# Kernel optimization log

Hardware: AMD Instinct MI355X
Metric: run time of the kernel (lower is better)

The kernel has to match this reference:

```python
import jax, jax.numpy as jnp
import numpy as np

N = 100000
E = 1600000
D_IN = 128
D_H = 128


def setup_inputs() -> dict:
    key = jax.random.key(0)
    ks = jax.random.split(key, 8)
    x = jax.random.normal(ks[0], (N, D_IN), dtype=jnp.float32)
    edge_index = jax.random.randint(ks[1], (2, E), 0, N, dtype=jnp.int64)
    edge_weights = jax.random.uniform(ks[2], (E,), dtype=jnp.float32)
    # GCNConv params (glorot-ish scale), bias zeros like PyG default init reset
    W1 = jax.random.normal(ks[3], (D_IN, D_H), dtype=jnp.float32) / np.sqrt(D_IN)
    b1 = jnp.zeros((D_H,), dtype=jnp.float32)
    W2 = jax.random.normal(ks[4], (D_H, D_H), dtype=jnp.float32) / np.sqrt(D_H)
    b2 = jnp.zeros((D_H,), dtype=jnp.float32)
    a_prelu = jnp.full((D_H,), 0.25, dtype=jnp.float32)  # nn.PReLU(hidden_dim)
    return {"x": x, "edge_index": edge_index, "edge_weights": edge_weights,
            "W1": W1, "b1": b1, "W2": W2, "b2": b2, "a_prelu": a_prelu}


def _gcn_norm(edge_index, edge_weights, n_nodes):
    # add self loops (weight 1), symmetric normalization deg^-1/2 A deg^-1/2
    loop = jnp.arange(n_nodes, dtype=edge_index.dtype)
    src = jnp.concatenate([edge_index[0], loop])
    dst = jnp.concatenate([edge_index[1], loop])
    w = jnp.concatenate([edge_weights, jnp.ones((n_nodes,), edge_weights.dtype)])
    deg = jax.ops.segment_sum(w, dst, num_segments=n_nodes)
    dis = jnp.where(deg > 0, jax.lax.rsqrt(jnp.maximum(deg, 1e-12)), 0.0)
    norm = dis[src] * w * dis[dst]
    return src, dst, norm


def _gcn_layer(h, W, b, src, dst, norm, n_nodes):
    h = h @ W                                   # [N, D] linear (no bias)
    msg = h[src] * norm[:, None]                # gather + scale  [E+N, D]
    out = jax.ops.segment_sum(msg, dst, num_segments=n_nodes)
    return out + b


def _prelu(z, a):
    return jnp.where(z >= 0, z, a * z)


def reference(x, edge_index, edge_weights, W1, b1, W2, b2, a_prelu):
    n = x.shape[0]
    src, dst, norm = _gcn_norm(edge_index, edge_weights, n)
    z = _prelu(_gcn_layer(x, W1, b1, src, dst, norm, n), a_prelu)
    z = _prelu(_gcn_layer(z, W2, b2, src, dst, norm, n), a_prelu)
    return z
```

## Files before the change

kernel.cpp:

```cpp
#include <hip/hip_runtime.h>
#include <hip/hip_fp16.h>

#define D 128
#define CAP 64
#define NBKT 512
#define CHUNK 4096
#define BKTCAP 5120

typedef _Float16 f16x8 __attribute__((ext_vector_type(8)));
typedef float f32x4 __attribute__((ext_vector_type(4)));

__global__ __launch_bounds__(256) void k_conv(const float2* __restrict__ X,
        const float* __restrict__ dis, __half2* __restrict__ Xh, int m) {
    int i = blockIdx.x * 256 + threadIdx.x;
    if (i < m) {
        float dv = dis[i >> 6];
        float2 f = X[i];
        Xh[i] = __floats2half2_rn(dv * f.x, dv * f.y);
    }
}

__global__ __launch_bounds__(256) void k_bin(const int* __restrict__ ei,
        const float* __restrict__ ew, int* __restrict__ gcur,
        int2* __restrict__ gbkt, int e) {
    __shared__ int hist[NBKT];
    __shared__ int base[NBKT];
    int t = threadIdx.x;
    int b0 = blockIdx.x * CHUNK;
    int cnt = min(CHUNK, e - b0);
    for (int i = t; i < NBKT; i += 256) hist[i] = 0;
    __syncthreads();
    int meta[16]; float w[16]; int pos[16]; int bkt[16];
    #pragma unroll
    for (int j = 0; j < 16; ++j) {
        int li = t + j * 256;
        bkt[j] = -1;
        if (li < cnt) {
            int i = b0 + li;
            int d = ei[e + i];
            int s = ei[i];
            bkt[j] = d >> 8;
            meta[j] = s | ((d & 255) << 24);
            w[j] = ew[i];
            pos[j] = atomicAdd(&hist[bkt[j]], 1);
        }
    }
    __syncthreads();
    for (int i = t; i < NBKT; i += 256)
        if (hist[i] > 0) base[i] = atomicAdd(&gcur[i], hist[i]);
    __syncthreads();
    #pragma unroll
    for (int j = 0; j < 16; ++j) {
        if (bkt[j] >= 0) {
            int idx = base[bkt[j]] + pos[j];
            if (idx < BKTCAP)
                gbkt[(size_t)bkt[j] * BKTCAP + idx] =
                    make_int2(meta[j], __float_as_int(w[j]));
        }
    }
}

__global__ __launch_bounds__(256) void k_scat2(const int2* __restrict__ gbkt,
        const int* __restrict__ gcur, int* cursor, int2* __restrict__ slot,
        float* __restrict__ dis, int n) {
    int bkt = blockIdx.x;
    int nodebase = bkt << 8;
    if (nodebase >= n) return;
    int cnt = min(gcur[bkt], BKTCAP);
    int t = threadIdx.x;
    for (int i = t; i < cnt; i += 256) {
        int2 r = gbkt[(size_t)bkt * BKTCAP + i];
        int d = nodebase | ((unsigned)r.x >> 24);
        int s = r.x & 0xFFFFFF;
        int pos = atomicAdd(&cursor[d], 1);
        if (pos < CAP) slot[(size_t)d * CAP + pos] = make_int2(s, r.y);
    }
    __syncthreads();
    int v = nodebase + t;
    if (v < n) {
        int c = min(atomicAdd(&cursor[v], 0), CAP);
        const int2* row = slot + (size_t)v * CAP;
        float wsum = 0.f;
        for (int i = 0; i < c; ++i) wsum += __int_as_float(row[i].y);
        dis[v] = rsqrtf(1.0f + wsum);
    }
}

__global__ __launch_bounds__(256) void k_agg(const __half2* __restrict__ Hs,
        const int2* __restrict__ slot, const int* __restrict__ cursor,
        const float* __restrict__ dis, __half2* __restrict__ out, int n) {
    int wid = threadIdx.x >> 6, lane = threadIdx.x & 63;
    int v = blockIdx.x * 4 + wid;
    if (v >= n) return;
    int half = lane >> 5;
    int m = lane & 31;
    int c = min(cursor[v], CAP);
    int c1 = c + 1;
    const int2* row = slot + (size_t)v * CAP;
    const __half* Hb = (const __half*)Hs;

    float4 acc = make_float4(0.f, 0.f, 0.f, 0.f);
    for (int i = 0; i < c1; i += 8) {
        int2 e[4];
        #pragma unroll
        for (int k = 0; k < 4; ++k) {
            int j = i + 2 * k + half;
            int jj = j - 1;
            jj = (jj < 0) ? 0 : (jj >= CAP ? CAP - 1 : jj);
            int2 ld = row[jj];
            bool real = (j >= 1) && (j < c1);
            int2 ee;
            ee.x = real ? (ld.x & 0xFFFFFF) : v;
            ee.y = real ? ld.y : ((j == 0) ? 0x3f800000 : 0);
            e[k] = ee;
        }
        float2 g[4];
        #pragma unroll
        for (int k = 0; k < 4; ++k)
            g[k] = *(const float2*)(Hb + ((size_t)e[k].x << 7) + (m << 2));
        #pragma unroll
        for (int k = 0; k < 4; ++k) {
            float w = __int_as_float(e[k].y);
            union { float2 f; __half2 h[2]; } u; u.f = g[k];
            float2 lo = __half22float2(u.h[0]);
            float2 hi = __half22float2(u.h[1]);
            acc.x = fmaf(w, lo.x, acc.x);
            acc.y = fmaf(w, lo.y, acc.y);
            acc.z = fmaf(w, hi.x, acc.z);
            acc.w = fmaf(w, hi.y, acc.w);
        }
    }
    acc.x += __shfl_xor(acc.x, 32);
    acc.y += __shfl_xor(acc.y, 32);
    acc.z += __shfl_xor(acc.z, 32);
    acc.w += __shfl_xor(acc.w, 32);
    if (half == 0) {
        float dv = dis[v];
        union { float2 f; __half2 h[2]; } o;
        o.h[0] = __floats2half2_rn(dv * acc.x, dv * acc.y);
        o.h[1] = __floats2half2_rn(dv * acc.z, dv * acc.w);
        *(float2*)((__half*)out + ((size_t)v << 7) + (m << 2)) = o.f;
    }
}

__global__ __launch_bounds__(256) void k_packW(const float* __restrict__ W,
        __half* __restrict__ Wpk) {
    int idx = blockIdx.x * 256 + threadIdx.x;
    if (idx >= 2048) return;
    int lane = idx & 63, nt = (idx >> 6) & 7, ks = idx >> 9;
    int col = nt * 16 + (lane & 15);
    int kb = ks * 32 + (lane >> 4) * 8;
    #pragma unroll
    for (int j = 0; j < 8; ++j)
        Wpk[idx * 8 + j] = __float2half(W[(kb + j) * D + col]);
}

template <bool HALF_OUT>
__global__ __launch_bounds__(256) void k_gemm(const __half* __restrict__ A,
        const __half* __restrict__ Wpk, const float* __restrict__ b,
        const float* __restrict__ ap, const float* __restrict__ dis,
        void* __restrict__ Cv, int n) {
    int t = threadIdx.x;
    int wv = t >> 6, lane = t & 63;
    int base = blockIdx.x * 64 + wv * 16;
    int row = base + (lane & 15);
    int rowc = min(row, n - 1);
    int kg = lane >> 4;

    const f16x8* Arow = (const f16x8*)(A + (size_t)rowc * D);
    f16x8 afr[4];
    #pragma unroll
    for (int ks = 0; ks < 4; ++ks) afr[ks] = Arow[ks * 4 + kg];

    const f16x8* Wp = (const f16x8*)Wpk;
    f32x4 acc[8];
    #pragma unroll
    for (int nt = 0; nt < 8; ++nt) acc[nt] = (f32x4){0.f, 0.f, 0.f, 0.f};

    #pragma unroll
    for (int ks = 0; ks < 4; ++ks) {
        #pragma unroll
        for (int nt = 0; nt < 8; ++nt) {
            f16x8 bfr = Wp[(ks * 8 + nt) * 64 + lane];
            acc[nt] = __builtin_amdgcn_mfma_f32_16x16x32_f16(afr[ks], bfr, acc[nt], 0, 0, 0);
        }
    }

    int c0 = lane & 15;
    int r0 = base + (lane >> 4) * 4;
    float dv[4];
    #pragma unroll
    for (int q = 0; q < 4; ++q)
        dv[q] = HALF_OUT ? dis[min(r0 + q, n - 1)] : 1.0f;
    #pragma unroll
    for (int nt = 0; nt < 8; ++nt) {
        int col = nt * 16 + c0;
        float bb = b[col], aa = ap[col];
        #pragma unroll
        for (int q = 0; q < 4; ++q) {
            int r = r0 + q;
            if (r < n) {
                float z = acc[nt][q] + bb;
                z = (z >= 0.f) ? z : aa * z;
                if (HALF_OUT) ((__half*)Cv)[(size_t)r * D + col] = __float2half(dv[q] * z);
                else          ((float*)Cv)[(size_t)r * D + col] = z;
            }
        }
    }
}


extern "C" void kernel_launch(void* const* d_in, const int* in_sizes, int n_in,
                              void* d_out, int out_size, void* d_ws, size_t ws_size,
                              hipStream_t stream) {
    const float* x  = (const float*)d_in[0];
    const int*   ei = (const int*)d_in[1];
    const float* ew = (const float*)d_in[2];
    const float* W1 = (const float*)d_in[3];
    const float* b1 = (const float*)d_in[4];
    const float* W2 = (const float*)d_in[5];
    const float* b2 = (const float*)d_in[6];
    const float* ap = (const float*)d_in[7];

    int n = in_sizes[0] / D;
    int e = in_sizes[2];

    int*     cursor = (int*)d_ws;
    int*     gcur   = cursor + n;
    float*   dis    = (float*)(gcur + NBKT);
    int2*    gbkt   = (int2*)(dis + n);
    int2*    slot   = gbkt + (size_t)NBKT * BKTCAP;
    __half2* xh     = (__half2*)(slot + (size_t)n * CAP);
    __half2* ah     = xh + (size_t)n * 64;
    __half*  Wpk1   = (__half*)(ah + (size_t)n * 64);
    __half*  Wpk2   = Wpk1 + 16384;
    float*   out    = (float*)d_out;

    int nbw = (n + 3) / 4;
    int nbg = (n + 63) / 64;
    int nbin = (e + CHUNK - 1) / CHUNK;

    hipMemsetAsync(cursor, 0, (size_t)(n + NBKT) * sizeof(int), stream);
    k_bin<<<nbin, 256, 0, stream>>>(ei, ew, gcur, gbkt, e);
    k_scat2<<<NBKT, 256, 0, stream>>>(gbkt, gcur, cursor, slot, dis, n);
    k_conv<<<(n * 64 + 255) / 256, 256, 0, stream>>>((const float2*)x, dis, xh, n * 64);
    k_packW<<<8, 256, 0, stream>>>(W1, Wpk1);
    k_packW<<<8, 256, 0, stream>>>(W2, Wpk2);

    k_agg<<<nbw, 256, 0, stream>>>(xh, slot, cursor, dis, ah, n);
    k_gemm<true><<<nbg, 256, 0, stream>>>((const __half*)ah, Wpk1, b1, ap, dis, (void*)xh, n);
    k_agg<<<nbw, 256, 0, stream>>>(xh, slot, cursor, dis, ah, n);
    k_gemm<false><<<nbg, 256, 0, stream>>>((const __half*)ah, Wpk2, b2, ap, dis, (void*)out, n);
}
```

Baseline: 265.8 us.

## Fuse neighbor aggregation into GEMM via LDS and compact packed CSR metadata

Aggregation and the MFMA GEMM now run in one kernel: each wave aggregates 16 rows into an LDS tile and feeds that tile straight to the MFMA, so the intermediate aggregated matrix no longer makes a round trip through global memory. The scatter kernel also builds a compact CSR-style array of 4-byte entries (17-bit source plus fp16 weight) using a block prefix scan, replacing the 8-byte padded slots. Edge metadata is loaded once per row and broadcast with shuffles. The cost is lower per-row parallelism in the gather loop, a 17-bit node-index limit, weights rounded to fp16, and the degree cap lowered to 62.

```diff
diff --git a/kernel.cpp b/kernel.cpp
--- a/kernel.cpp
+++ b/kernel.cpp
@@ -62,7 +62,9 @@
 
 __global__ __launch_bounds__(256) void k_scat2(const int2* __restrict__ gbkt,
         const int* __restrict__ gcur, int* cursor, int2* __restrict__ slot,
+        unsigned* __restrict__ meta, int* __restrict__ rsc,
         float* __restrict__ dis, int n) {
+    __shared__ int sscan[256];
     int bkt = blockIdx.x;
     int nodebase = bkt << 8;
     if (nodebase >= n) return;
@@ -77,69 +79,33 @@
     }
     __syncthreads();
     int v = nodebase + t;
+    int c = 0;
     if (v < n) {
-        int c = min(atomicAdd(&cursor[v], 0), CAP);
+        c = min(atomicAdd(&cursor[v], 0), 62);
         const int2* row = slot + (size_t)v * CAP;
         float wsum = 0.f;
         for (int i = 0; i < c; ++i) wsum += __int_as_float(row[i].y);
         dis[v] = rsqrtf(1.0f + wsum);
     }
-}
-
-__global__ __launch_bounds__(256) void k_agg(const __half2* __restrict__ Hs,
-        const int2* __restrict__ slot, const int* __restrict__ cursor,
-        const float* __restrict__ dis, __half2* __restrict__ out, int n) {
-    int wid = threadIdx.x >> 6, lane = threadIdx.x & 63;
-    int v = blockIdx.x * 4 + wid;
-    if (v >= n) return;
-    int half = lane >> 5;
-    int m = lane & 31;
-    int c = min(cursor[v], CAP);
-    int c1 = c + 1;
-    const int2* row = slot + (size_t)v * CAP;
-    const __half* Hb = (const __half*)Hs;
-
-    float4 acc = make_float4(0.f, 0.f, 0.f, 0.f);
-    for (int i = 0; i < c1; i += 8) {
-        int2 e[4];
-        #pragma unroll
-        for (int k = 0; k < 4; ++k) {
-            int j = i + 2 * k + half;
-            int jj = j - 1;
-            jj = (jj < 0) ? 0 : (jj >= CAP ? CAP - 1 : jj);
-            int2 ld = row[jj];
-            bool real = (j >= 1) && (j < c1);
-            int2 ee;
-            ee.x = real ? (ld.x & 0xFFFFFF) : v;
-            ee.y = real ? ld.y : ((j == 0) ? 0x3f800000 : 0);
-            e[k] = ee;
-        }
-        float2 g[4];
-        #pragma unroll
-        for (int k = 0; k < 4; ++k)
-            g[k] = *(const float2*)(Hb + ((size_t)e[k].x << 7) + (m << 2));
-        #pragma unroll
-        for (int k = 0; k < 4; ++k) {
-            float w = __int_as_float(e[k].y);
-            union { float2 f; __half2 h[2]; } u; u.f = g[k];
-            float2 lo = __half22float2(u.h[0]);
-            float2 hi = __half22float2(u.h[1]);
-            acc.x = fmaf(w, lo.x, acc.x);
-            acc.y = fmaf(w, lo.y, acc.y);
-            acc.z = fmaf(w, hi.x, acc.z);
-            acc.w = fmaf(w, hi.y, acc.w);
-        }
-    }
-    acc.x += __shfl_xor(acc.x, 32);
-    acc.y += __shfl_xor(acc.y, 32);
-    acc.z += __shfl_xor(acc.z, 32);
-    acc.w += __shfl_xor(acc.w, 32);
-    if (half == 0) {
-        float dv = dis[v];
-        union { float2 f; __half2 h[2]; } o;
-        o.h[0] = __floats2half2_rn(dv * acc.x, dv * acc.y);
-        o.h[1] = __floats2half2_rn(dv * acc.z, dv * acc.w);
-        *(float2*)((__half*)out + ((size_t)v << 7) + (m << 2)) = o.f;
+    sscan[t] = c;
+    __syncthreads();
+    int val = c;
+    for (int off = 1; off < 256; off <<= 1) {
+        int tmp = (t >= off) ? sscan[t - off] : 0;
+        __syncthreads();
+        sscan[t] += tmp;
+        __syncthreads();
+    }
+    if (v < n) {
+        int myoff = sscan[t] - val;
+        int mb = bkt * BKTCAP + myoff;
+        rsc[v] = mb | (c << 24);
+        const int2* row = slot + (size_t)v * CAP;
+        for (int i = 0; i < c; ++i) {
+            int2 sw = row[i];
+            unsigned hb = (unsigned)__half_as_ushort(__float2half(__int_as_float(sw.y)));
+            meta[mb + i] = (unsigned)sw.x | (hb << 17);
+        }
     }
 }
 
@@ -156,27 +122,74 @@
 }
 
 template <bool HALF_OUT>
-__global__ __launch_bounds__(256) void k_gemm(const __half* __restrict__ A,
-        const __half* __restrict__ Wpk, const float* __restrict__ b,
-        const float* __restrict__ ap, const float* __restrict__ dis,
+__global__ __launch_bounds__(256) void k_fused(const __half* __restrict__ Hs,
+        const unsigned* __restrict__ meta, const int* __restrict__ rsc,
+        const float* __restrict__ dis, const __half* __restrict__ Wpk,
+        const float* __restrict__ bias, const float* __restrict__ ap,
         void* __restrict__ Cv, int n) {
-    int t = threadIdx.x;
-    int wv = t >> 6, lane = t & 63;
+    __shared__ __half As[4][16][136];
+    int t = threadIdx.x, wv = t >> 6, lane = t & 63;
     int base = blockIdx.x * 64 + wv * 16;
-    int row = base + (lane & 15);
-    int rowc = min(row, n - 1);
+    int half = lane >> 5, m = lane & 31;
+    const char* Hb = (const char*)Hs;
+
+    for (int r = 0; r < 16; ++r) {
+        int v = base + r;
+        float4 a0 = make_float4(0.f, 0.f, 0.f, 0.f);
+        float4 a1 = make_float4(0.f, 0.f, 0.f, 0.f);
+        float dv = 0.f;
+        if (v < n) {
+            dv = dis[v];
+            int rc = rsc[v];
+            int rs = rc & 0xFFFFFF;
+            int c1 = (int)((unsigned)rc >> 24) + 1;
+            unsigned mm;
+            if (lane == 0) mm = (unsigned)v | (0x3C00u << 17);
+            else if (lane < c1) mm = meta[rs + lane - 1];
+            else mm = (unsigned)v;
+            int voff = (int)(mm & 0x1FFFFu) << 8;
+            float wf = __half2float(__ushort_as_half((unsigned short)(mm >> 17)));
+            for (int j0 = 0; j0 < c1; j0 += 4) {
+                int sl0 = j0 + half, sl1 = j0 + 2 + half;
+                int vo0 = __shfl(voff, sl0);
+                float w0 = __shfl(wf, sl0);
+                int vo1 = __shfl(voff, sl1);
+                float w1 = __shfl(wf, sl1);
+                float2 g0 = *(const float2*)(Hb + vo0 + (m << 3));
+                float2 g1 = *(const float2*)(Hb + vo1 + (m << 3));
+                union { float2 f; __half2 h[2]; } u0, u1;
+                u0.f = g0; u1.f = g1;
+                float2 l0 = __half22float2(u0.h[0]), h0 = __half22float2(u0.h[1]);
+                float2 l1 = __half22float2(u1.h[0]), h1 = __half22float2(u1.h[1]);
+                a0.x = fmaf(w0, l0.x, a0.x); a0.y = fmaf(w0, l0.y, a0.y);
+                a0.z = fmaf(w0, h0.x, a0.z); a0.w = fmaf(w0, h0.y, a0.w);
+                a1.x = fmaf(w1, l1.x, a1.x); a1.y = fmaf(w1, l1.y, a1.y);
+                a1.z = fmaf(w1, h1.x, a1.z); a1.w = fmaf(w1, h1.y, a1.w);
+            }
+        }
+        a0.x += a1.x; a0.y += a1.y; a0.z += a1.z; a0.w += a1.w;
+        a0.x += __shfl_xor(a0.x, 32);
+        a0.y += __shfl_xor(a0.y, 32);
+        a0.z += __shfl_xor(a0.z, 32);
+        a0.w += __shfl_xor(a0.w, 32);
+        if (half == 0) {
+            union { float2 f; __half2 h[2]; } o;
+            o.h[0] = __floats2half2_rn(dv * a0.x, dv * a0.y);
+            o.h[1] = __floats2half2_rn(dv * a0.z, dv * a0.w);
+            *(float2*)(&As[wv][r][m << 2]) = o.f;
+        }
+    }
+
     int kg = lane >> 4;
-
-    const f16x8* Arow = (const f16x8*)(A + (size_t)rowc * D);
     f16x8 afr[4];
     #pragma unroll
-    for (int ks = 0; ks < 4; ++ks) afr[ks] = Arow[ks * 4 + kg];
+    for (int ks = 0; ks < 4; ++ks)
+        afr[ks] = *(const f16x8*)(&As[wv][lane & 15][ks * 32 + kg * 8]);
 
     const f16x8* Wp = (const f16x8*)Wpk;
     f32x4 acc[8];
     #pragma unroll
     for (int nt = 0; nt < 8; ++nt) acc[nt] = (f32x4){0.f, 0.f, 0.f, 0.f};
-
     #pragma unroll
     for (int ks = 0; ks < 4; ++ks) {
         #pragma unroll
@@ -195,7 +208,7 @@
     #pragma unroll
     for (int nt = 0; nt < 8; ++nt) {
         int col = nt * 16 + c0;
-        float bb = b[col], aa = ap[col];
+        float bb = bias[col], aa = ap[col];
         #pragma unroll
         for (int q = 0; q < 4; ++q) {
             int r = r0 + q;
@@ -225,30 +238,31 @@
     int n = in_sizes[0] / D;
     int e = in_sizes[2];
 
-    int*     cursor = (int*)d_ws;
-    int*     gcur   = cursor + n;
-    float*   dis    = (float*)(gcur + NBKT);
-    int2*    gbkt   = (int2*)(dis + n);
-    int2*    slot   = gbkt + (size_t)NBKT * BKTCAP;
-    __half2* xh     = (__half2*)(slot + (size_t)n * CAP);
-    __half2* ah     = xh + (size_t)n * 64;
-    __half*  Wpk1   = (__half*)(ah + (size_t)n * 64);
-    __half*  Wpk2   = Wpk1 + 16384;
-    float*   out    = (float*)d_out;
-
-    int nbw = (n + 3) / 4;
+    int*      cursor = (int*)d_ws;
+    int*      gcur   = cursor + n;
+    float*    dis    = (float*)(gcur + NBKT);
+    int*      rsc    = (int*)(dis + n);
+    int2*     gbkt   = (int2*)(rsc + n);
+    int2*     slot   = gbkt + (size_t)NBKT * BKTCAP;
+    unsigned* meta   = (unsigned*)(slot + (size_t)n * CAP);
+    __half2*  xh     = (__half2*)(meta + (size_t)NBKT * BKTCAP);
+    __half2*  z1h    = xh + (size_t)n * 64;
+    __half*   Wpk1   = (__half*)(z1h + (size_t)n * 64);
+    __half*   Wpk2   = Wpk1 + 16384;
+    float*    out    = (float*)d_out;
+
+    int nbin = (e + CHUNK - 1) / CHUNK;
     int nbg = (n + 63) / 64;
-    int nbin = (e + CHUNK - 1) / CHUNK;
 
     hipMemsetAsync(cursor, 0, (size_t)(n + NBKT) * sizeof(int), stream);
     k_bin<<<nbin, 256, 0, stream>>>(ei, ew, gcur, gbkt, e);
-    k_scat2<<<NBKT, 256, 0, stream>>>(gbkt, gcur, cursor, slot, dis, n);
+    k_scat2<<<NBKT, 256, 0, stream>>>(gbkt, gcur, cursor, slot, meta, rsc, dis, n);
     k_conv<<<(n * 64 + 255) / 256, 256, 0, stream>>>((const float2*)x, dis, xh, n * 64);
     k_packW<<<8, 256, 0, stream>>>(W1, Wpk1);
     k_packW<<<8, 256, 0, stream>>>(W2, Wpk2);
 
-    k_agg<<<nbw, 256, 0, stream>>>(xh, slot, cursor, dis, ah, n);
-    k_gemm<true><<<nbg, 256, 0, stream>>>((const __half*)ah, Wpk1, b1, ap, dis, (void*)xh, n);
-    k_agg<<<nbw, 256, 0, stream>>>(xh, slot, cursor, dis, ah, n);
-    k_gemm<false><<<nbg, 256, 0, stream>>>((const __half*)ah, Wpk2, b2, ap, dis, (void*)out, n);
-}
+    k_fused<true><<<nbg, 256, 0, stream>>>((const __half*)xh, meta, rsc, dis,
+                                           Wpk1, b1, ap, (void*)z1h, n);
+    k_fused<false><<<nbg, 256, 0, stream>>>((const __half*)z1h, meta, rsc, dis,
+                                            Wpk2, b2, ap, (void*)out, n);
+}
```

Result: slower. 310.8 us (+16.9%).

## Replace fixed-capacity per-node slots with compact CSR built in-block, fuse conversion

Applied to the files above, without the earlier changes.

Rebuilds the per-bucket scatter so that each block histograms its 256 destination nodes in shared memory, prefix-scans the counts, and writes edges into a compact CSR-like array packed with a row offset and count per node. This replaces the fixed 64-slot per-node layout and its global atomics and per-node memset. Degree-weight sums are accumulated in shared memory, and the fp16 conversion of x is folded into the same kernel. The two weight-pack launches are merged into one, and layer-1 output now goes to a separate buffer. Counts are clamped at 255, and the gather in aggregation becomes more compact and cache friendly.

```diff
diff --git a/kernel.cpp b/kernel.cpp
--- a/kernel.cpp
+++ b/kernel.cpp
@@ -2,23 +2,12 @@
 #include <hip/hip_fp16.h>
 
 #define D 128
-#define CAP 64
 #define NBKT 512
 #define CHUNK 4096
 #define BKTCAP 5120
 
 typedef _Float16 f16x8 __attribute__((ext_vector_type(8)));
 typedef float f32x4 __attribute__((ext_vector_type(4)));
-
-__global__ __launch_bounds__(256) void k_conv(const float2* __restrict__ X,
-        const float* __restrict__ dis, __half2* __restrict__ Xh, int m) {
-    int i = blockIdx.x * 256 + threadIdx.x;
-    if (i < m) {
-        float dv = dis[i >> 6];
-        float2 f = X[i];
-        Xh[i] = __floats2half2_rn(dv * f.x, dv * f.y);
-    }
-}
 
 __global__ __launch_bounds__(256) void k_bin(const int* __restrict__ ei,
         const float* __restrict__ ew, int* __restrict__ gcur,
@@ -61,42 +50,76 @@
 }
 
 __global__ __launch_bounds__(256) void k_scat2(const int2* __restrict__ gbkt,
-        const int* __restrict__ gcur, int* cursor, int2* __restrict__ slot,
-        float* __restrict__ dis, int n) {
+        const int* __restrict__ gcur, const float2* __restrict__ X,
+        int2* __restrict__ meta, int* __restrict__ rsc, float* __restrict__ dis,
+        __half2* __restrict__ xh, int n) {
+    __shared__ int hist[256];
+    __shared__ int cur[256];
+    __shared__ int scn[256];
+    __shared__ int basearr[256];
+    __shared__ float wsum[256];
+    __shared__ float disv[256];
     int bkt = blockIdx.x;
     int nodebase = bkt << 8;
-    if (nodebase >= n) return;
+    int t = threadIdx.x;
     int cnt = min(gcur[bkt], BKTCAP);
-    int t = threadIdx.x;
+    hist[t] = 0; cur[t] = 0; wsum[t] = 0.f;
+    __syncthreads();
     for (int i = t; i < cnt; i += 256) {
         int2 r = gbkt[(size_t)bkt * BKTCAP + i];
-        int d = nodebase | ((unsigned)r.x >> 24);
-        int s = r.x & 0xFFFFFF;
-        int pos = atomicAdd(&cursor[d], 1);
-        if (pos < CAP) slot[(size_t)d * CAP + pos] = make_int2(s, r.y);
-    }
-    __syncthreads();
+        int dl = (unsigned)r.x >> 24;
+        atomicAdd(&hist[dl], 1);
+        atomicAdd(&wsum[dl], __int_as_float(r.y));
+    }
+    __syncthreads();
+    int c = hist[t];
+    scn[t] = c;
+    __syncthreads();
+    for (int off = 1; off < 256; off <<= 1) {
+        int tmp = (t >= off) ? scn[t - off] : 0;
+        __syncthreads();
+        scn[t] += tmp;
+        __syncthreads();
+    }
+    int myoff = scn[t] - c;
+    basearr[t] = myoff;
+    __syncthreads();
+    for (int i = t; i < cnt; i += 256) {
+        int2 r = gbkt[(size_t)bkt * BKTCAP + i];
+        int dl = (unsigned)r.x >> 24;
+        int pos = atomicAdd(&cur[dl], 1);
+        meta[(size_t)bkt * BKTCAP + basearr[dl] + pos] =
+            make_int2(r.x & 0xFFFFFF, r.y);
+    }
     int v = nodebase + t;
+    float dv = 1.f;
     if (v < n) {
-        int c = min(atomicAdd(&cursor[v], 0), CAP);
-        const int2* row = slot + (size_t)v * CAP;
-        float wsum = 0.f;
-        for (int i = 0; i < c; ++i) wsum += __int_as_float(row[i].y);
-        dis[v] = rsqrtf(1.0f + wsum);
+        dv = rsqrtf(1.0f + wsum[t]);
+        dis[v] = dv;
+        rsc[v] = (bkt * BKTCAP + myoff) | (min(c, 255) << 24);
+    }
+    disv[t] = dv;
+    __syncthreads();
+    int nrow = min(256, n - nodebase);
+    size_t rowbase = (size_t)nodebase << 6;
+    for (int idx = t; idx < nrow * 64; idx += 256) {
+        float dv2 = disv[idx >> 6];
+        float2 f = X[rowbase + idx];
+        xh[rowbase + idx] = __floats2half2_rn(dv2 * f.x, dv2 * f.y);
     }
 }
 
 __global__ __launch_bounds__(256) void k_agg(const __half2* __restrict__ Hs,
-        const int2* __restrict__ slot, const int* __restrict__ cursor,
+        const int2* __restrict__ meta, const int* __restrict__ rsc,
         const float* __restrict__ dis, __half2* __restrict__ out, int n) {
     int wid = threadIdx.x >> 6, lane = threadIdx.x & 63;
     int v = blockIdx.x * 4 + wid;
     if (v >= n) return;
     int half = lane >> 5;
     int m = lane & 31;
-    int c = min(cursor[v], CAP);
-    int c1 = c + 1;
-    const int2* row = slot + (size_t)v * CAP;
+    int rc = rsc[v];
+    int c1 = (int)((unsigned)rc >> 24) + 1;
+    const int2* row = meta + (rc & 0xFFFFFF);
     const __half* Hb = (const __half*)Hs;
 
     float4 acc = make_float4(0.f, 0.f, 0.f, 0.f);
@@ -106,11 +129,11 @@
         for (int k = 0; k < 4; ++k) {
             int j = i + 2 * k + half;
             int jj = j - 1;
-            jj = (jj < 0) ? 0 : (jj >= CAP ? CAP - 1 : jj);
+            jj = (jj < 0) ? 0 : jj;
             int2 ld = row[jj];
             bool real = (j >= 1) && (j < c1);
             int2 ee;
-            ee.x = real ? (ld.x & 0xFFFFFF) : v;
+            ee.x = real ? ld.x : v;
             ee.y = real ? ld.y : ((j == 0) ? 0x3f800000 : 0);
             e[k] = ee;
         }
@@ -143,16 +166,20 @@
     }
 }
 
-__global__ __launch_bounds__(256) void k_packW(const float* __restrict__ W,
-        __half* __restrict__ Wpk) {
-    int idx = blockIdx.x * 256 + threadIdx.x;
-    if (idx >= 2048) return;
+__global__ __launch_bounds__(256) void k_packW(const float* __restrict__ W1,
+        const float* __restrict__ W2, __half* __restrict__ Wpk1,
+        __half* __restrict__ Wpk2) {
+    int gidx = blockIdx.x * 256 + threadIdx.x;
+    if (gidx >= 4096) return;
+    const float* W = (gidx < 2048) ? W1 : W2;
+    __half* P = (gidx < 2048) ? Wpk1 : Wpk2;
+    int idx = gidx & 2047;
     int lane = idx & 63, nt = (idx >> 6) & 7, ks = idx >> 9;
     int col = nt * 16 + (lane & 15);
     int kb = ks * 32 + (lane >> 4) * 8;
     #pragma unroll
     for (int j = 0; j < 8; ++j)
-        Wpk[idx * 8 + j] = __float2half(W[(kb + j) * D + col]);
+        P[idx * 8 + j] = __float2half(W[(kb + j) * D + col]);
 }
 
 template <bool HALF_OUT>
@@ -225,30 +252,30 @@
     int n = in_sizes[0] / D;
     int e = in_sizes[2];
 
-    int*     cursor = (int*)d_ws;
-    int*     gcur   = cursor + n;
-    float*   dis    = (float*)(gcur + NBKT);
-    int2*    gbkt   = (int2*)(dis + n);
-    int2*    slot   = gbkt + (size_t)NBKT * BKTCAP;
-    __half2* xh     = (__half2*)(slot + (size_t)n * CAP);
-    __half2* ah     = xh + (size_t)n * 64;
-    __half*  Wpk1   = (__half*)(ah + (size_t)n * 64);
-    __half*  Wpk2   = Wpk1 + 16384;
-    float*   out    = (float*)d_out;
-
-    int nbw = (n + 3) / 4;
-    int nbg = (n + 63) / 64;
+    int*     gcur = (int*)d_ws;
+    float*   dis  = (float*)(gcur + NBKT);
+    int*     rsc  = (int*)(dis + n);
+    int2*    gbkt = (int2*)(rsc + n);
+    int2*    meta = gbkt + (size_t)NBKT * BKTCAP;
+    __half2* xh   = (__half2*)(meta + (size_t)NBKT * BKTCAP + 256);
+    __half2* z1h  = xh + (size_t)n * 64;
+    __half2* ah   = z1h + (size_t)n * 64;
+    __half*  Wpk1 = (__half*)(ah + (size_t)n * 64);
+    __half*  Wpk2 = Wpk1 + 16384;
+    float*   out  = (float*)d_out;
+
     int nbin = (e + CHUNK - 1) / CHUNK;
-
-    hipMemsetAsync(cursor, 0, (size_t)(n + NBKT) * sizeof(int), stream);
+    int nbb  = (n + 255) / 256;
+    int nbw  = (n + 3) / 4;
+    int nbg  = (n + 63) / 64;
+
+    hipMemsetAsync(gcur, 0, NBKT * sizeof(int), stream);
+    k_packW<<<16, 256, 0, stream>>>(W1, W2, Wpk1, Wpk2);
     k_bin<<<nbin, 256, 0, stream>>>(ei, ew, gcur, gbkt, e);
-    k_scat2<<<NBKT, 256, 0, stream>>>(gbkt, gcur, cursor, slot, dis, n);
-    k_conv<<<(n * 64 + 255) / 256, 256, 0, stream>>>((const float2*)x, dis, xh, n * 64);
-    k_packW<<<8, 256, 0, stream>>>(W1, Wpk1);
-    k_packW<<<8, 256, 0, stream>>>(W2, Wpk2);
-
-    k_agg<<<nbw, 256, 0, stream>>>(xh, slot, cursor, dis, ah, n);
-    k_gemm<true><<<nbg, 256, 0, stream>>>((const __half*)ah, Wpk1, b1, ap, dis, (void*)xh, n);
-    k_agg<<<nbw, 256, 0, stream>>>(xh, slot, cursor, dis, ah, n);
+    k_scat2<<<nbb, 256, 0, stream>>>(gbkt, gcur, (const float2*)x, meta, rsc, dis, xh, n);
+
+    k_agg<<<nbw, 256, 0, stream>>>(xh, meta, rsc, dis, ah, n);
+    k_gemm<true><<<nbg, 256, 0, stream>>>((const __half*)ah, Wpk1, b1, ap, dis, (void*)z1h, n);
+    k_agg<<<nbw, 256, 0, stream>>>(z1h, meta, rsc, dis, ah, n);
     k_gemm<false><<<nbg, 256, 0, stream>>>((const __half*)ah, Wpk2, b2, ap, dis, (void*)out, n);
 }
```

Measured after the change: 250.4 us. 1.06x faster.
